# Kernel tuning notes

Measured on AMD Instinct MI355X. Metric: run time of the kernel, lower is better.

## Reference

```python
import jax, jax.numpy as jnp
import numpy as np

CAPACITY_FACTOR = 1.2


def setup_inputs() -> dict:
    key = jax.random.key(0)
    k1, k2, k3 = jax.random.split(key, 3)
    B, S, D, E = 8, 4096, 512, 16
    x = jax.random.normal(k1, (B, S, D), dtype=jnp.float32)
    switch_w = jax.random.normal(k2, (E, D), dtype=jnp.float32) * 0.02
    switch_b = jnp.zeros((E,), dtype=jnp.float32)
    expert_w = jax.random.normal(k3, (E, D, D), dtype=jnp.float32) * 0.02
    expert_b = jnp.zeros((E, D), dtype=jnp.float32)
    return {"x": x, "switch_w": switch_w, "switch_b": switch_b,
            "expert_w": expert_w, "expert_b": expert_b}


def reference(x, switch_w, switch_b, expert_w, expert_b):
    B, S, D = x.shape
    E = switch_w.shape[0]
    N = B * S
    xf = x.reshape(N, D)

    # Router: softmax over experts, top-1 route.
    logits = xf @ switch_w.T + switch_b            # [N, E]
    probs = jax.nn.softmax(logits, axis=-1)
    route_probs = jnp.max(probs, axis=-1)          # [N]
    routes = jnp.argmax(probs, axis=-1)            # [N] int

    # Position of each token within its expert's queue (token order).
    oh = jax.nn.one_hot(routes, E, dtype=jnp.int32)            # [N, E]
    pos = jnp.take_along_axis(jnp.cumsum(oh, axis=0), routes[:, None], axis=1)[:, 0] - 1  # [N]

    capacity = int(CAPACITY_FACTOR * N / E)        # static
    keep = pos < capacity                          # [N] bool; overflow tokens dropped

    # Dispatch: scatter kept tokens into [E, capacity, D] buffer.
    # Out-of-capacity positions are out-of-bounds and dropped by scatter semantics.
    buf = jnp.zeros((E, capacity, D), dtype=xf.dtype).at[routes, pos].set(xf)

    # Per-expert Linear (torch Linear: y = x @ W.T + b), as one grouped GEMM.
    y = jnp.einsum('ecd,efd->ecf', buf, expert_w) + expert_b[:, None, :]  # [E, C, D]

    # Combine: gather expert outputs back; dropped tokens pass through x.
    gathered = y[routes, jnp.minimum(pos, capacity - 1)]       # [N, D]
    out = jnp.where(keep[:, None], gathered, xf) * route_probs[:, None]
    return out.reshape(B, S, D)
```

## Files before the change

kernel.cpp:

```cpp
#include <hip/hip_runtime.h>
#include <math.h>

#define N_TOK 32768
#define DIM   512
#define NEXP  16
#define CAP   2457
#define CAPP  2464
#define NCHUNK 512

typedef __attribute__((ext_vector_type(8))) short   short8;
typedef __attribute__((ext_vector_type(4))) short   short4v;
typedef __attribute__((ext_vector_type(4))) float   floatx4;

__device__ __forceinline__ short f2bf(float f) {
  unsigned u = __builtin_bit_cast(unsigned, f);
  unsigned r = u + 0x7FFFu + ((u >> 16) & 1u);
  return (short)(r >> 16);
}
__device__ __forceinline__ float bf2f(short h) {
  return __builtin_bit_cast(float, ((unsigned)(unsigned short)h) << 16);
}

#define LGP 17
__global__ __launch_bounds__(256) void router_k(
    const float* __restrict__ x, const float* __restrict__ sw,
    const float* __restrict__ sb, const float* __restrict__ ew,
    int* __restrict__ route, float* __restrict__ prob, int* __restrict__ hist,
    short* __restrict__ x_bf, short* __restrict__ w_bf) {
  __shared__ short swh[16][520];
  __shared__ short swl[16][520];
  __shared__ float lgt[64][LGP];
  __shared__ float sbs[NEXP];

  int tid = threadIdx.x;

  {
    const float4* src = (const float4*)ew;
    short4v* dst = (short4v*)w_bf;
    int base = blockIdx.x * 2048 + tid;
#pragma unroll
    for (int i = 0; i < 8; ++i) {
      float4 f = src[base + i * 256];
      short4v s;
      s[0] = f2bf(f.x); s[1] = f2bf(f.y); s[2] = f2bf(f.z); s[3] = f2bf(f.w);
      dst[base + i * 256] = s;
    }
  }

  {
    int idx = tid;
#pragma unroll
    for (int i = 0; i < 8; ++i, idx += 256) {
      int e = idx >> 7, k4 = idx & 127;
      float4 f = ((const float4*)(sw + e * DIM))[k4];
      short4v h, l;
      h[0] = f2bf(f.x); h[1] = f2bf(f.y); h[2] = f2bf(f.z); h[3] = f2bf(f.w);
      l[0] = f2bf(f.x - bf2f(h[0]));
      l[1] = f2bf(f.y - bf2f(h[1]));
      l[2] = f2bf(f.z - bf2f(h[2]));
      l[3] = f2bf(f.w - bf2f(h[3]));
      *(short4v*)&swh[e][k4 * 4] = h;
      *(short4v*)&swl[e][k4 * 4] = l;
    }
  }
  if (tid < NEXP) sbs[tid] = sb[tid];
  __syncthreads();

  int wv = tid >> 6, lane = tid & 63, q = lane >> 4, l16 = lane & 15;
  int row = blockIdx.x * 64 + wv * 16 + l16;
  const float* xr = x + (size_t)row * DIM;
  short* xbr = x_bf + (size_t)row * DIM;

  floatx4 acc = {};
#pragma unroll 4
  for (int kc = 0; kc < 16; ++kc) {
    int k0 = kc * 32 + q * 8;
    float4 f0 = *(const float4*)(xr + k0);
    float4 f1 = *(const float4*)(xr + k0 + 4);
    short8 hi, lo;
    hi[0] = f2bf(f0.x); hi[1] = f2bf(f0.y); hi[2] = f2bf(f0.z); hi[3] = f2bf(f0.w);
    hi[4] = f2bf(f1.x); hi[5] = f2bf(f1.y); hi[6] = f2bf(f1.z); hi[7] = f2bf(f1.w);
    lo[0] = f2bf(f0.x - bf2f(hi[0])); lo[1] = f2bf(f0.y - bf2f(hi[1]));
    lo[2] = f2bf(f0.z - bf2f(hi[2])); lo[3] = f2bf(f0.w - bf2f(hi[3]));
    lo[4] = f2bf(f1.x - bf2f(hi[4])); lo[5] = f2bf(f1.y - bf2f(hi[5]));
    lo[6] = f2bf(f1.z - bf2f(hi[6])); lo[7] = f2bf(f1.w - bf2f(hi[7]));
    *(short8*)(xbr + k0) = hi;
    short8 bh = *(const short8*)&swh[l16][k0];
    short8 bl = *(const short8*)&swl[l16][k0];
    acc = __builtin_amdgcn_mfma_f32_16x16x32_bf16(hi, bh, acc, 0, 0, 0);
    acc = __builtin_amdgcn_mfma_f32_16x16x32_bf16(lo, bh, acc, 0, 0, 0);
    acc = __builtin_amdgcn_mfma_f32_16x16x32_bf16(hi, bl, acc, 0, 0, 0);
    acc = __builtin_amdgcn_mfma_f32_16x16x32_bf16(lo, bl, acc, 0, 0, 0);
  }
#pragma unroll
  for (int r = 0; r < 4; ++r)
    lgt[wv * 16 + q * 4 + r][l16] = acc[r];
  __syncthreads();

  if (tid < 64) {
    int t = blockIdx.x * 64 + tid;
    float lg[NEXP];
#pragma unroll
    for (int e = 0; e < NEXP; ++e) lg[e] = lgt[tid][e] + sbs[e];
    int arg = 0; float mx = lg[0];
#pragma unroll
    for (int e = 1; e < NEXP; ++e)
      if (lg[e] > mx) { mx = lg[e]; arg = e; }
    float s = 0.f;
#pragma unroll
    for (int e = 0; e < NEXP; ++e) s += expf(lg[e] - mx);
    route[t] = arg;
    prob[t]  = 1.0f / s;
#pragma unroll
    for (int e = 0; e < NEXP; ++e) {
      unsigned long long m = __ballot(arg == e);
      if (tid == e) hist[blockIdx.x * NEXP + e] = __popcll(m);
    }
  }
}

__global__ __launch_bounds__(256) void pos_k(
    const int* __restrict__ route, const float* __restrict__ prob,
    const int* __restrict__ hist, const float* __restrict__ x,
    float* __restrict__ out, int* __restrict__ lists,
    int* __restrict__ counts) {
  __shared__ int part[16][NEXP];
  __shared__ int base_s[NEXP];
  __shared__ int wcnt[4][NEXP];
  int tid = threadIdx.x;
  int b = blockIdx.x;
  int c0 = b * 4;
  {
    int g = tid >> 4, e = tid & 15;
    int s = 0;
    for (int c = g; c < c0; c += 16) s += hist[c * NEXP + e];
    part[g][e] = s;
  }
  __syncthreads();
  if (tid < NEXP) {
    int s = 0;
#pragma unroll
    for (int gg = 0; gg < 16; ++gg) s += part[gg][tid];
    base_s[tid] = s;
  }
  int wv = tid >> 6, lane = tid & 63;
  int t = b * 256 + wv * 64 + lane;
  int r = route[t];
  unsigned long long lower = (1ull << lane) - 1ull;
  int rank = 0;
#pragma unroll
  for (int e = 0; e < NEXP; ++e) {
    unsigned long long m = __ballot(r == e);
    if (r == e) rank = __popcll(m & lower);
    if (lane == e) wcnt[wv][e] = __popcll(m);
  }
  __syncthreads();
  int pre = base_s[r];
  for (int w2 = 0; w2 < wv; ++w2) pre += wcnt[w2][r];
  int pos = pre + rank;
  if (pos < CAP) {
    lists[r * CAPP + pos] = t;
  } else {
    float p = prob[t];
    const float4* xr = (const float4*)(x + (size_t)t * DIM);
    float4* o = (float4*)(out + (size_t)t * DIM);
    for (int d = 0; d < DIM / 4; ++d) {
      float4 v = xr[d];
      v.x *= p; v.y *= p; v.z *= p; v.w *= p;
      o[d] = v;
    }
  }
  if (b == 127 && tid < NEXP)
    counts[tid] = base_s[tid] + wcnt[0][tid] + wcnt[1][tid]
                + wcnt[2][tid] + wcnt[3][tid];
}

#define BM 64
#define BN 128
#define BKS 64

__global__ __launch_bounds__(256, 4) void gemm_k(
    const short* __restrict__ x_bf, const short* __restrict__ w_bf,
    const float* __restrict__ eb, const int* __restrict__ lists,
    const int* __restrict__ counts, const float* __restrict__ prob,
    float* __restrict__ out) {
  int e = blockIdx.z;
  int cnt = counts[e]; if (cnt > CAP) cnt = CAP;
  int row0 = blockIdx.y * BM;
  if (row0 >= cnt) return;
  int col0 = blockIdx.x * BN;

  __shared__ short A_s[BM * BKS];
  __shared__ short B_s[BN * BKS];
  __shared__ int rowtok[BM];

  int tid = threadIdx.x;
  if (tid < BM) {
    int gr = row0 + tid;
    rowtok[tid] = (gr < cnt) ? lists[e * CAPP + gr] : 0;
  }
  __syncthreads();

  int wv = tid >> 6, lane = tid & 63;
  int q = lane >> 4, l16 = lane & 15;
  int wrow = (wv >> 1) * 32, wcol = (wv & 1) * 64;

  int r_loc = lane >> 3, c = lane & 7;
  const short* ga[2]; short* la[2];
  const short* gb[4]; short* lb[4];
#pragma unroll
  for (int t2 = 0; t2 < 2; ++t2) {
    int row = wv * 16 + t2 * 8 + r_loc;
    int g = c ^ (row & 7);
    ga[t2] = x_bf + (size_t)rowtok[row] * DIM + g * 8;
    la[t2] = &A_s[(wv * 16 + t2 * 8) * BKS];
  }
#pragma unroll
  for (int t4 = 0; t4 < 4; ++t4) {
    int row = wv * 32 + t4 * 8 + r_loc;
    int g = c ^ (row & 7);
    gb[t4] = w_bf + (size_t)(e * DIM + col0 + row) * DIM + g * 8;
    lb[t4] = &B_s[(wv * 32 + t4 * 8) * BKS];
  }

  floatx4 acc[2][4] = {};

  for (int k0 = 0; k0 < DIM; k0 += BKS) {
#pragma unroll
    for (int t2 = 0; t2 < 2; ++t2)
      __builtin_amdgcn_global_load_lds(
          (const __attribute__((address_space(1))) void*)(ga[t2] + k0),
          (__attribute__((address_space(3))) void*)(la[t2]), 16, 0, 0);
#pragma unroll
    for (int t4 = 0; t4 < 4; ++t4)
      __builtin_amdgcn_global_load_lds(
          (const __attribute__((address_space(1))) void*)(gb[t4] + k0),
          (__attribute__((address_space(3))) void*)(lb[t4]), 16, 0, 0);
    __syncthreads();
#pragma unroll
    for (int kk = 0; kk < 2; ++kk) {
      short8 af[2], bfv[4];
      int ckbase = kk * 4 + q;
#pragma unroll
      for (int sm = 0; sm < 2; ++sm) {
        int row = wrow + sm * 16 + l16;
        int ph = ckbase ^ (row & 7);
        af[sm] = *(const short8*)&A_s[row * BKS + ph * 8];
      }
#pragma unroll
      for (int sn = 0; sn < 4; ++sn) {
        int row = wcol + sn * 16 + l16;
        int ph = ckbase ^ (row & 7);
        bfv[sn] = *(const short8*)&B_s[row * BKS + ph * 8];
      }
#pragma unroll
      for (int sm = 0; sm < 2; ++sm)
#pragma unroll
        for (int sn = 0; sn < 4; ++sn)
          acc[sm][sn] = __builtin_amdgcn_mfma_f32_16x16x32_bf16(
              af[sm], bfv[sn], acc[sm][sn], 0, 0, 0);
    }
    __syncthreads();
  }

#pragma unroll
  for (int sm = 0; sm < 2; ++sm) {
    int tt[4]; float pp[4]; int vld[4];
#pragma unroll
    for (int rg = 0; rg < 4; ++rg) {
      int rr = wrow + sm * 16 + q * 4 + rg;
      int gr = row0 + rr;
      vld[rg] = (gr < cnt);
      tt[rg]  = rowtok[rr];
      pp[rg]  = vld[rg] ? prob[tt[rg]] : 0.f;
    }
#pragma unroll
    for (int sn = 0; sn < 4; ++sn) {
      int col = col0 + wcol + sn * 16 + l16;
      float bias = eb[e * DIM + col];
#pragma unroll
      for (int rg = 0; rg < 4; ++rg)
        if (vld[rg])
          out[(size_t)tt[rg] * DIM + col] = (acc[sm][sn][rg] + bias) * pp[rg];
    }
  }
}

extern "C" void kernel_launch(void* const* d_in, const int* in_sizes, int n_in,
                              void* d_out, int out_size, void* d_ws, size_t ws_size,
                              hipStream_t stream) {
  const float* x  = (const float*)d_in[0];
  const float* sw = (const float*)d_in[1];
  const float* sb = (const float*)d_in[2];
  const float* ew = (const float*)d_in[3];
  const float* eb = (const float*)d_in[4];
  float* out = (float*)d_out;

  char* ws = (char*)d_ws;
  int*   route  = (int*)(ws + 0);
  float* prob   = (float*)(ws + 131072);
  int*   hist   = (int*)(ws + 262144);
  int*   counts = (int*)(ws + 327680);
  int*   lists  = (int*)(ws + 327744);
  short* x_bf   = (short*)(ws + (1 << 20));
  short* w_bf   = (short*)(ws + (1 << 20) + 33554432);

  hipLaunchKernelGGL(router_k, dim3(NCHUNK), dim3(256), 0, stream,
                     x, sw, sb, ew, route, prob, hist, x_bf, w_bf);
  hipLaunchKernelGGL(pos_k, dim3(128), dim3(256), 0, stream,
                     route, prob, hist, x, out, lists, counts);
  hipLaunchKernelGGL(gemm_k, dim3(4, 39, 16), dim3(256), 0, stream,
                     x_bf, w_bf, eb, lists, counts, prob, out);
}
```

Before: 183.6 us.

## Widen GEMM tile to 64x256 and split router K across wave pairs

The grouped GEMM tile goes from 64x128 to 64x256. Each wave now computes all 64 rows against its own 64 columns, which halves the number of times each A tile (the gathered token rows) is reloaded and raises MFMA work per LDS fragment load. The router launches twice as many blocks with 32 tokens each, and two waves split the K reduction for every 16-row group. This spreads the bandwidth-heavy fp32-to-bf16 conversion across more blocks. The cost is higher register and LDS use per GEMM block, which may lower occupancy, and fewer GEMM blocks overall.

```diff
diff --git a/kernel.cpp b/kernel.cpp
--- a/kernel.cpp
+++ b/kernel.cpp
@@ -6,7 +6,7 @@
 #define NEXP  16
 #define CAP   2457
 #define CAPP  2464
-#define NCHUNK 512
+#define NCHUNK 1024
 
 typedef __attribute__((ext_vector_type(8))) short   short8;
 typedef __attribute__((ext_vector_type(4))) short   short4v;
@@ -29,7 +29,7 @@
     short* __restrict__ x_bf, short* __restrict__ w_bf) {
   __shared__ short swh[16][520];
   __shared__ short swl[16][520];
-  __shared__ float lgt[64][LGP];
+  __shared__ float lgt[4][16][LGP];
   __shared__ float sbs[NEXP];
 
   int tid = threadIdx.x;
@@ -37,9 +37,9 @@
   {
     const float4* src = (const float4*)ew;
     short4v* dst = (short4v*)w_bf;
-    int base = blockIdx.x * 2048 + tid;
-#pragma unroll
-    for (int i = 0; i < 8; ++i) {
+    int base = blockIdx.x * 1024 + tid;
+#pragma unroll
+    for (int i = 0; i < 4; ++i) {
       float4 f = src[base + i * 256];
       short4v s;
       s[0] = f2bf(f.x); s[1] = f2bf(f.y); s[2] = f2bf(f.z); s[3] = f2bf(f.w);
@@ -67,14 +67,15 @@
   __syncthreads();
 
   int wv = tid >> 6, lane = tid & 63, q = lane >> 4, l16 = lane & 15;
-  int row = blockIdx.x * 64 + wv * 16 + l16;
+  int pair = wv >> 1, half = wv & 1;
+  int row = blockIdx.x * 32 + pair * 16 + l16;
   const float* xr = x + (size_t)row * DIM;
   short* xbr = x_bf + (size_t)row * DIM;
 
   floatx4 acc = {};
-#pragma unroll 4
-  for (int kc = 0; kc < 16; ++kc) {
-    int k0 = kc * 32 + q * 8;
+#pragma unroll
+  for (int i = 0; i < 8; ++i) {
+    int k0 = (half * 8 + i) * 32 + q * 8;
     float4 f0 = *(const float4*)(xr + k0);
     float4 f1 = *(const float4*)(xr + k0 + 4);
     short8 hi, lo;
@@ -94,14 +95,16 @@
   }
 #pragma unroll
   for (int r = 0; r < 4; ++r)
-    lgt[wv * 16 + q * 4 + r][l16] = acc[r];
-  __syncthreads();
-
-  if (tid < 64) {
-    int t = blockIdx.x * 64 + tid;
+    lgt[wv][q * 4 + r][l16] = acc[r];
+  __syncthreads();
+
+  if (tid < 32) {
+    int t = blockIdx.x * 32 + tid;
+    int p = tid >> 4, tk = tid & 15;
     float lg[NEXP];
 #pragma unroll
-    for (int e = 0; e < NEXP; ++e) lg[e] = lgt[tid][e] + sbs[e];
+    for (int e = 0; e < NEXP; ++e)
+      lg[e] = lgt[p * 2][tk][e] + lgt[p * 2 + 1][tk][e] + sbs[e];
     int arg = 0; float mx = lg[0];
 #pragma unroll
     for (int e = 1; e < NEXP; ++e)
@@ -129,7 +132,7 @@
   __shared__ int wcnt[4][NEXP];
   int tid = threadIdx.x;
   int b = blockIdx.x;
-  int c0 = b * 4;
+  int c0 = b * 8;
   {
     int g = tid >> 4, e = tid & 15;
     int s = 0;
@@ -176,7 +179,7 @@
 }
 
 #define BM 64
-#define BN 128
+#define BN 256
 #define BKS 64
 
 __global__ __launch_bounds__(256, 4) void gemm_k(
@@ -203,11 +206,9 @@
 
   int wv = tid >> 6, lane = tid & 63;
   int q = lane >> 4, l16 = lane & 15;
-  int wrow = (wv >> 1) * 32, wcol = (wv & 1) * 64;
-
   int r_loc = lane >> 3, c = lane & 7;
+
   const short* ga[2]; short* la[2];
-  const short* gb[4]; short* lb[4];
 #pragma unroll
   for (int t2 = 0; t2 < 2; ++t2) {
     int row = wv * 16 + t2 * 8 + r_loc;
@@ -215,15 +216,16 @@
     ga[t2] = x_bf + (size_t)rowtok[row] * DIM + g * 8;
     la[t2] = &A_s[(wv * 16 + t2 * 8) * BKS];
   }
-#pragma unroll
-  for (int t4 = 0; t4 < 4; ++t4) {
-    int row = wv * 32 + t4 * 8 + r_loc;
+  const short* gb[8]; short* lb[8];
+#pragma unroll
+  for (int t8 = 0; t8 < 8; ++t8) {
+    int row = wv * 64 + t8 * 8 + r_loc;
     int g = c ^ (row & 7);
-    gb[t4] = w_bf + (size_t)(e * DIM + col0 + row) * DIM + g * 8;
-    lb[t4] = &B_s[(wv * 32 + t4 * 8) * BKS];
-  }
-
-  floatx4 acc[2][4] = {};
+    gb[t8] = w_bf + (size_t)(e * DIM + col0 + row) * DIM + g * 8;
+    lb[t8] = &B_s[(wv * 64 + t8 * 8) * BKS];
+  }
+
+  floatx4 acc[4][4] = {};
 
   for (int k0 = 0; k0 < DIM; k0 += BKS) {
 #pragma unroll
@@ -232,29 +234,29 @@
           (const __attribute__((address_space(1))) void*)(ga[t2] + k0),
           (__attribute__((address_space(3))) void*)(la[t2]), 16, 0, 0);
 #pragma unroll
-    for (int t4 = 0; t4 < 4; ++t4)
+    for (int t8 = 0; t8 < 8; ++t8)
       __builtin_amdgcn_global_load_lds(
-          (const __attribute__((address_space(1))) void*)(gb[t4] + k0),
-          (__attribute__((address_space(3))) void*)(lb[t4]), 16, 0, 0);
+          (const __attribute__((address_space(1))) void*)(gb[t8] + k0),
+          (__attribute__((address_space(3))) void*)(lb[t8]), 16, 0, 0);
     __syncthreads();
 #pragma unroll
     for (int kk = 0; kk < 2; ++kk) {
-      short8 af[2], bfv[4];
+      short8 af[4], bfv[4];
       int ckbase = kk * 4 + q;
 #pragma unroll
-      for (int sm = 0; sm < 2; ++sm) {
-        int row = wrow + sm * 16 + l16;
+      for (int sm = 0; sm < 4; ++sm) {
+        int row = sm * 16 + l16;
         int ph = ckbase ^ (row & 7);
         af[sm] = *(const short8*)&A_s[row * BKS + ph * 8];
       }
 #pragma unroll
       for (int sn = 0; sn < 4; ++sn) {
-        int row = wcol + sn * 16 + l16;
+        int row = wv * 64 + sn * 16 + l16;
         int ph = ckbase ^ (row & 7);
         bfv[sn] = *(const short8*)&B_s[row * BKS + ph * 8];
       }
 #pragma unroll
-      for (int sm = 0; sm < 2; ++sm)
+      for (int sm = 0; sm < 4; ++sm)
 #pragma unroll
         for (int sn = 0; sn < 4; ++sn)
           acc[sm][sn] = __builtin_amdgcn_mfma_f32_16x16x32_bf16(
@@ -264,11 +266,11 @@
   }
 
 #pragma unroll
-  for (int sm = 0; sm < 2; ++sm) {
+  for (int sm = 0; sm < 4; ++sm) {
     int tt[4]; float pp[4]; int vld[4];
 #pragma unroll
     for (int rg = 0; rg < 4; ++rg) {
-      int rr = wrow + sm * 16 + q * 4 + rg;
+      int rr = sm * 16 + q * 4 + rg;
       int gr = row0 + rr;
       vld[rg] = (gr < cnt);
       tt[rg]  = rowtok[rr];
@@ -276,7 +278,7 @@
     }
 #pragma unroll
     for (int sn = 0; sn < 4; ++sn) {
-      int col = col0 + wcol + sn * 16 + l16;
+      int col = col0 + wv * 64 + sn * 16 + l16;
       float bias = eb[e * DIM + col];
 #pragma unroll
       for (int rg = 0; rg < 4; ++rg)
@@ -309,6 +311,6 @@
                      x, sw, sb, ew, route, prob, hist, x_bf, w_bf);
   hipLaunchKernelGGL(pos_k, dim3(128), dim3(256), 0, stream,
                      route, prob, hist, x, out, lists, counts);
-  hipLaunchKernelGGL(gemm_k, dim3(4, 39, 16), dim3(256), 0, stream,
+  hipLaunchKernelGGL(gemm_k, dim3(2, 39, 16), dim3(256), 0, stream,
                      x_bf, w_bf, eb, lists, counts, prob, out);
 }
```

Result: slower. 191.9 us (+4.5%).
